# Performance work log

Measured on AMD Instinct MI355X. Metric: run time of the kernel, lower is better.

## Reference

```python
import jax, jax.numpy as jnp
import numpy as np

NUM_HEADS = 16
THETA = 10000.0


def _rope(x, cos, sin):
    # x: [B, H, S, d_k]; cos/sin: [S, d_k//2] broadcast over B, H
    x1 = x[..., 0::2]
    x2 = x[..., 1::2]
    r1 = cos * x1 - sin * x2
    r2 = sin * x1 + cos * x2
    # interleave back: (..., half_d, 2) -> (..., d_k)
    return jnp.stack((r1, r2), axis=-1).reshape(x.shape)


def setup_inputs() -> dict:
    key = jax.random.key(0)
    ks = jax.random.split(key, 5)
    B, S, D = 4, 2048, 1024
    scale = D ** -0.5
    x = jax.random.normal(ks[0], (B, S, D), dtype=jnp.float32)
    wq = jax.random.normal(ks[1], (D, D), dtype=jnp.float32) * scale
    wk = jax.random.normal(ks[2], (D, D), dtype=jnp.float32) * scale
    wv = jax.random.normal(ks[3], (D, D), dtype=jnp.float32) * scale
    wo = jax.random.normal(ks[4], (D, D), dtype=jnp.float32) * scale
    return {"x": x, "wq": wq, "wk": wk, "wv": wv, "wo": wo}


def reference(x, wq, wk, wv, wo):
    B, S, D = x.shape
    H = NUM_HEADS
    dk = D // H

    def proj(w):
        # x @ w.T, split heads -> [B, H, S, dk]
        y = jnp.einsum('bsd,ed->bse', x, w)
        return y.reshape(B, S, H, dk).transpose(0, 2, 1, 3)

    q, k, v = proj(wq), proj(wk), proj(wv)

    # RoPE (interleaved pairs), positions = arange(S)
    inv_freq = THETA ** (-(jnp.arange(0, dk, 2, dtype=jnp.float32) / dk))
    ang = jnp.arange(S, dtype=jnp.float32)[:, None] * inv_freq  # [S, dk//2]
    cos, sin = jnp.cos(ang), jnp.sin(ang)
    q = _rope(q, cos, sin)
    k = _rope(k, cos, sin)

    scores = jnp.einsum('bhqd,bhkd->bhqk', q, k) / jnp.sqrt(jnp.asarray(dk, x.dtype))
    causal = jnp.tril(jnp.ones((S, S), dtype=bool))  # keep self + past
    scores = jnp.where(causal, scores, -jnp.inf)
    p = jax.nn.softmax(scores, axis=-1)
    attn = jnp.einsum('bhqk,bhkd->bhqd', p, v)
    attn = attn.transpose(0, 2, 1, 3).reshape(B, S, D)
    return jnp.einsum('bsd,ed->bse', attn, wo)
```

## Files before the change

### kernel.cpp

```cpp
#include <hip/hip_runtime.h>
#include <hip/hip_bf16.h>
#include <cstdint>
#include <cstddef>

#define Bb 4
#define Ss 2048
#define Dd 1024
#define Hh 16
#define Mm (Bb*Ss)

typedef __bf16 bf16_t;
typedef __bf16 bf16x8 __attribute__((ext_vector_type(8)));
typedef __bf16 bf16x4 __attribute__((ext_vector_type(4)));
typedef float  f32x4  __attribute__((ext_vector_type(4)));
typedef float  f32x16 __attribute__((ext_vector_type(16)));
typedef unsigned int u32x4 __attribute__((ext_vector_type(4)));
typedef unsigned int u32x2 __attribute__((ext_vector_type(2)));

#define MFMA16(a,b,c) __builtin_amdgcn_mfma_f32_16x16x32_bf16(a,b,c,0,0,0)
#define MFMA32(a,b,c) __builtin_amdgcn_mfma_f32_32x32x16_bf16(a,b,c,0,0,0)

#define QSCALE 0.18033688011112042f

static __device__ __forceinline__ float fexp2(float x) {
#if __has_builtin(__builtin_amdgcn_exp2f)
  return __builtin_amdgcn_exp2f(x);
#else
  return exp2f(x);
#endif
}

static __device__ __forceinline__ bf16x8 ld16g(const bf16_t* p) {
  return __builtin_bit_cast(bf16x8, *reinterpret_cast<const u32x4*>(p));
}

static __device__ __forceinline__ void gload_lds16(const bf16_t* g, bf16_t* l) {
  __builtin_amdgcn_global_load_lds(
      (__attribute__((address_space(1))) void*)(g),
      (__attribute__((address_space(3))) void*)(l),
      16, 0, 0);
}

__global__ void prep_k(const float* __restrict__ x,  const float* __restrict__ wq,
                       const float* __restrict__ wk, const float* __restrict__ wv,
                       const float* __restrict__ wo,
                       bf16_t* __restrict__ xb, bf16_t* __restrict__ wqkv,
                       float2* __restrict__ tab) {
  int bid = blockIdx.x;
  if (bid < 8192) {
    int i = (bid * 256 + threadIdx.x) * 4;
    float4 f = *reinterpret_cast<const float4*>(x + i);
    xb[i + 0] = (bf16_t)f.x; xb[i + 1] = (bf16_t)f.y;
    xb[i + 2] = (bf16_t)f.z; xb[i + 3] = (bf16_t)f.w;
  } else if (bid < 12288) {
    int b2 = bid - 8192;
    int seg = b2 >> 10, local = b2 & 1023;
    const float* w = (seg == 0) ? wq : (seg == 1) ? wk : (seg == 2) ? wv : wo;
    int i = (local * 256 + threadIdx.x) * 4;
    float4 f = *reinterpret_cast<const float4*>(w + i);
    bf16_t* o = wqkv + (size_t)seg * (Dd * Dd) + i;
    o[0] = (bf16_t)f.x; o[1] = (bf16_t)f.y; o[2] = (bf16_t)f.z; o[3] = (bf16_t)f.w;
  } else {
    int idx = (bid - 12288) * 256 + threadIdx.x;
    int i = idx & 31, s = idx >> 5;
    float inv_freq = exp2f(-(float)i * (13.2877123795494f / 32.0f));
    float ang = (float)s * inv_freq;
    float sn, cs;
    sincosf(ang, &sn, &cs);
    tab[idx] = make_float2(cs, sn);
  }
}

template <typename OutT>
__global__ __launch_bounds__(256, 3) void gemm_r3(const bf16_t* __restrict__ A,
                                                  const bf16_t* __restrict__ Bm,
                                                  OutT* __restrict__ C0,
                                                  OutT* __restrict__ C1,
                                                  OutT* __restrict__ C2,
                                                  const float2* __restrict__ tab,
                                                  int Kdim) {
  __shared__ bf16_t As[3][128 * 32];
  __shared__ bf16_t Bs[3][128 * 32];
  const int t = threadIdx.x;
  const int lane = t & 63, w = t >> 6;
  const int l15 = lane & 15, lg = lane >> 4;
  const int wr = w >> 1, wc = w & 1;
  const int m0 = blockIdx.x * 128, n0 = blockIdx.y * 128;

  const bf16_t* gA[2];
  const bf16_t* gB[2];
#pragma unroll
  for (int i = 0; i < 2; ++i) {
    int q = i * 256 + t, row = q >> 2, sl = (q & 3) ^ ((row >> 1) & 3);
    gA[i] = A  + (size_t)(m0 + row) * Kdim + sl * 8;
    gB[i] = Bm + (size_t)(n0 + row) * Kdim + sl * 8;
  }
  const int wb = w * 64 * 8;

  auto stage = [&](int slot, int k0) {
#pragma unroll
    for (int i = 0; i < 2; ++i) {
      gload_lds16(gA[i] + k0, &As[slot][i * 2048 + wb]);
      gload_lds16(gB[i] + k0, &Bs[slot][i * 2048 + wb]);
    }
  };

  int aoff[4], boff[4];
#pragma unroll
  for (int i = 0; i < 4; ++i) {
    int row = wr * 64 + i * 16 + l15;
    aoff[i] = row * 32 + ((lg ^ ((row >> 1) & 3)) * 8);
  }
#pragma unroll
  for (int j = 0; j < 4; ++j) {
    int row = wc * 64 + j * 16 + l15;
    boff[j] = row * 32 + ((lg ^ ((row >> 1) & 3)) * 8);
  }

  f32x4 acc[4][4] = {};
  const int KT = Kdim / 32;

  stage(0, 0);
  stage(1, 32);
  for (int j = 0; j < KT; ++j) {
    if (j == KT - 1) {
      asm volatile("s_waitcnt vmcnt(0) lgkmcnt(0)" ::: "memory");
    } else {
      asm volatile("s_waitcnt vmcnt(4) lgkmcnt(0)" ::: "memory");
    }
    __builtin_amdgcn_s_barrier();
    if (j + 2 < KT) stage((j + 2) % 3, (j + 2) * 32);
    const bf16_t* ab = As[j % 3];
    const bf16_t* bb = Bs[j % 3];
    bf16x8 a[4], b[4];
#pragma unroll
    for (int jj = 0; jj < 4; ++jj)
      b[jj] = __builtin_bit_cast(bf16x8,
               *reinterpret_cast<const u32x4*>(bb + boff[jj]));
#pragma unroll
    for (int i = 0; i < 4; ++i)
      a[i] = __builtin_bit_cast(bf16x8,
               *reinterpret_cast<const u32x4*>(ab + aoff[i]));
    __builtin_amdgcn_s_setprio(1);
#pragma unroll
    for (int i = 0; i < 4; ++i)
#pragma unroll
      for (int jj = 0; jj < 4; ++jj)
        acc[i][jj] = MFMA16(a[i], b[jj], acc[i][jj]);
    __builtin_amdgcn_s_setprio(0);
  }

  OutT* Cs = (n0 < 1024) ? C0 : (n0 < 2048 ? C1 : C2);
  const int nb = n0 & 1023;
  const bool doRope = (tab != nullptr) && (n0 < 2048);
  const float qs = (n0 < 1024) ? QSCALE : 1.0f;

  if (doRope) {
#pragma unroll
    for (int i = 0; i < 4; ++i) {
      int rowb = m0 + wr * 64 + i * 16 + lg * 4;
#pragma unroll
      for (int j = 0; j < 4; ++j) {
        int col = nb + wc * 64 + j * 16 + l15;
        int i0 = (col & 63) >> 1;
        const bool ev = !(col & 1);
#pragma unroll
        for (int r = 0; r < 4; ++r) {
          float v = acc[i][j][r];
          float px = __shfl_xor(v, 1);
          int s = (rowb + r) & (Ss - 1);
          float2 f = tab[s * 32 + i0];
          float sn = ev ? -f.y : f.y;
          Cs[(size_t)(rowb + r) * 1024 + col] = (OutT)((f.x * v + sn * px) * qs);
        }
      }
    }
  } else {
#pragma unroll
    for (int i = 0; i < 4; ++i) {
      int rowb = m0 + wr * 64 + i * 16 + lg * 4;
#pragma unroll
      for (int j = 0; j < 4; ++j) {
        int col = nb + wc * 64 + j * 16 + l15;
#pragma unroll
        for (int r = 0; r < 4; ++r)
          Cs[(size_t)(rowb + r) * 1024 + col] = (OutT)acc[i][j][r];
      }
    }
  }
}

__global__ __launch_bounds__(256) void transpose_v(const bf16_t* __restrict__ V,
                                                   bf16_t* __restrict__ Vt) {
  __shared__ bf16_t tile[64][72];
  int bh = blockIdx.y;
  int b = bh >> 4, h = bh & 15;
  int s0 = blockIdx.x * 64;
  int t = threadIdx.x;
  const bf16_t* vbase = V + (size_t)b * Ss * Dd + h * 64;
#pragma unroll
  for (int c = 0; c < 2; ++c) {
    int cf = c * 256 + t;
    int s = cf >> 3, d8 = cf & 7;
    u32x4 v = *reinterpret_cast<const u32x4*>(vbase + (size_t)(s0 + s) * Dd + d8 * 8);
    *reinterpret_cast<u32x4*>(&tile[s][d8 * 8]) = v;
  }
  __syncthreads();
  bf16_t* obase = Vt + (size_t)bh * 64 * Ss;
#pragma unroll
  for (int c = 0; c < 2; ++c) {
    int cf = c * 256 + t;
    int d = cf >> 3, s8 = cf & 7;
    __align__(16) bf16_t tmp[8];
#pragma unroll
    for (int i = 0; i < 8; ++i) tmp[i] = tile[s8 * 8 + i][d];
    *reinterpret_cast<u32x4*>(obase + (size_t)d * Ss + s0 + s8 * 8) =
        *reinterpret_cast<const u32x4*>(tmp);
  }
}

__global__ __launch_bounds__(256, 2) void attn_k(const bf16_t* __restrict__ Q,
                                                 const bf16_t* __restrict__ K,
                                                 const bf16_t* __restrict__ Vt,
                                                 bf16_t* __restrict__ O) {
  __shared__ bf16_t Ks[3][4096];
  __shared__ bf16_t Vs[3][4096];
  const int t = threadIdx.x, lane = t & 63, w = t >> 6;
  const int l31 = lane & 31, hi = lane >> 5, hi8 = hi * 8;
  const int bh = blockIdx.y, b = bh >> 4, h = bh & 15;
  const int bx = blockIdx.x;
  const int i = bx * 4 + w;
  const int q0a = 32 * i, q0b = 2016 - 32 * i;
  const int dtA = q0a >> 6, hfA = (q0a >> 5) & 1;
  const int dtB = q0b >> 6, hfB = (q0b >> 5) & 1;
  const int NT = 32 - 2 * bx;
  const bf16_t* qb = Q + (size_t)b * Ss * Dd + h * 64;
  const bf16_t* kb = K + (size_t)b * Ss * Dd + h * 64;
  const bf16_t* vtb = Vt + (size_t)bh * 64 * Ss;

  const int a_ = l31 >> 2, c_ = l31 & 3;
  const int tau = (a_ >> 1) + 2 * (a_ & 1) + ((a_ & 4) >> 1);
  const int sig = c_ + 4 * tau;

  int kfoff[4];
#pragma unroll
  for (int c = 0; c < 4; ++c) {
    int j = sig >> 1, u = (sig & 1) * 8 + c * 2 + hi;
    kfoff[c] = j * 128 + ((u ^ j) * 8);
  }
  int vfoff[2][2];
#pragma unroll
  for (int db = 0; db < 2; ++db)
#pragma unroll
    for (int ks = 0; ks < 2; ++ks) {
      int d = db * 32 + l31, j = d >> 2, u = (d & 3) * 4 + ks * 2 + hi;
      vfoff[db][ks] = j * 128 + ((u ^ j) * 8);
    }

  const int sj = t >> 4, ss = t & 15, su = ss ^ sj;
  const bf16_t* ksrc0 = kb + (size_t)(2 * sj + (su >> 3)) * Dd + (su & 7) * 8;
  const bf16_t* vsrc0 = vtb + (size_t)(4 * sj + (su >> 2)) * Ss + (su & 3) * 8;

  auto stage = [&](int buf, int kb0) {
    bf16_t* kd = &Ks[buf][w * 512];
    bf16_t* vd = &Vs[buf][w * 512];
    gload_lds16(ksrc0 + (size_t)kb0 * Dd, kd);
    gload_lds16(ksrc0 + (size_t)(kb0 + 32) * Dd, kd + 2048);
    gload_lds16(vsrc0 + kb0, vd);
    gload_lds16(vsrc0 + kb0 + 32, vd + 2048);
  };

  bf16x8 qf[2][4];
#pragma unroll
  for (int c = 0; c < 4; ++c) {
    qf[0][c] = ld16g(qb + (size_t)(q0a + l31) * Dd + c * 16 + hi8);
    qf[1][c] = ld16g(qb + (size_t)(q0b + l31) * Dd + c * 16 + hi8);
  }

  float l_[2] = {0.f, 0.f};
  f32x16 o_[2][2] = {};

  auto chain = [&](int kt, int dt, int hf, bf16x8 (&qc)[4],
                   f32x16& o0, f32x16& o1, float& lc,
                   bf16x8 (&kf)[2][4], bf16x8 (&vf)[2][2][2]) {
    if (kt > dt) return;
    const bool last = (kt == dt);
    const bool do1 = !(last && hf == 0);
    f32x16 s0 = {}, s1 = {};
    __builtin_amdgcn_s_setprio(1);
    s0 = MFMA32(kf[0][0], qc[0], s0);
    s0 = MFMA32(kf[0][1], qc[1], s0);
    s0 = MFMA32(kf[0][2], qc[2], s0);
    s0 = MFMA32(kf[0][3], qc[3], s0);
    if (do1) {
      s1 = MFMA32(kf[1][0], qc[0], s1);
      s1 = MFMA32(kf[1][1], qc[1], s1);
      s1 = MFMA32(kf[1][2], qc[2], s1);
      s1 = MFMA32(kf[1][3], qc[3], s1);
    }
    __builtin_amdgcn_s_setprio(0);
    if (last) {
      if (hf) {
#pragma unroll
        for (int reg = 0; reg < 16; ++reg) {
          const int koff = (reg & 3) + 4 * (reg >> 2) + 8 * ((reg >> 2) >> 1) + hi8;
          s1[reg] = (koff <= l31) ? s1[reg] : -INFINITY;
        }
      } else {
#pragma unroll
        for (int reg = 0; reg < 16; ++reg) {
          const int koff = (reg & 3) + 4 * (reg >> 2) + 8 * ((reg >> 2) >> 1) + hi8;
          s0[reg] = (koff <= l31) ? s0[reg] : -INFINITY;
        }
      }
    }
    float p0[16], p1[16];
#pragma unroll
    for (int r = 0; r < 16; ++r) p0[r] = fexp2(s0[r]);
    bf16x8 pa0, pa1, pb0, pb1;
#pragma unroll
    for (int r = 0; r < 8; ++r) { pa0[r] = (bf16_t)p0[r]; pa1[r] = (bf16_t)p0[r + 8]; }
    if (do1) {
#pragma unroll
      for (int r = 0; r < 16; ++r) p1[r] = fexp2(s1[r]);
#pragma unroll
      for (int r = 0; r < 8; ++r) { pb0[r] = (bf16_t)p1[r]; pb1[r] = (bf16_t)p1[r + 8]; }
#pragma unroll
      for (int r = 0; r < 16; ++r) p0[r] += p1[r];
    }
#pragma unroll
    for (int st2 = 8; st2 > 0; st2 >>= 1)
#pragma unroll
      for (int r = 0; r < st2; ++r) p0[r] += p0[r + st2];
    lc += p0[0];
    __builtin_amdgcn_s_setprio(1);
    o0 = MFMA32(vf[0][0][0], pa0, o0);
    o0 = MFMA32(vf[0][0][1], pa1, o0);
    o1 = MFMA32(vf[0][1][0], pa0, o1);
    o1 = MFMA32(vf[0][1][1], pa1, o1);
    if (do1) {
      o0 = MFMA32(vf[1][0][0], pb0, o0);
      o0 = MFMA32(vf[1][0][1], pb1, o0);
      o1 = MFMA32(vf[1][1][0], pb0, o1);
      o1 = MFMA32(vf[1][1][1], pb1, o1);
    }
    __builtin_amdgcn_s_setprio(0);
  };

  stage(0, 0);
  stage(1, 64);
  for (int j = 0; j < NT; ++j) {
    if (j == NT - 1) {
      asm volatile("s_waitcnt vmcnt(0) lgkmcnt(0)" ::: "memory");
    } else {
      asm volatile("s_waitcnt vmcnt(4) lgkmcnt(0)" ::: "memory");
    }
    __builtin_amdgcn_s_barrier();
    if (j + 2 < NT) stage((j + 2) % 3, (j + 2) * 64);
    const bf16_t* kbuf = &Ks[j % 3][0];
    const bf16_t* vbuf = &Vs[j % 3][0];
    bf16x8 kf[2][4], vf[2][2][2];
#pragma unroll
    for (int st = 0; st < 2; ++st)
#pragma unroll
      for (int c = 0; c < 4; ++c)
        kf[st][c] = __builtin_bit_cast(bf16x8,
            *reinterpret_cast<const u32x4*>(kbuf + st * 2048 + kfoff[c]));
#pragma unroll
    for (int st = 0; st < 2; ++st)
#pragma unroll
      for (int db = 0; db < 2; ++db)
#pragma unroll
        for (int ks = 0; ks < 2; ++ks)
          vf[st][db][ks] = __builtin_bit_cast(bf16x8,
              *reinterpret_cast<const u32x4*>(vbuf + st * 2048 + vfoff[db][ks]));
    chain(j, dtA, hfA, qf[0], o_[0][0], o_[0][1], l_[0], kf, vf);
    chain(j, dtB, hfB, qf[1], o_[1][0], o_[1][1], l_[1], kf, vf);
  }

#pragma unroll
  for (int ch = 0; ch < 2; ++ch) {
    const float ltot = l_[ch] + __shfl_xor(l_[ch], 32);
    const float inv = 1.0f / ltot;
    const size_t rowoff = ((size_t)b * Ss + (ch ? q0b : q0a) + l31) * Dd + h * 64;
#pragma unroll
    for (int db = 0; db < 2; ++db)
#pragma unroll
      for (int tt = 0; tt < 4; ++tt) {
        bf16x4 ov;
#pragma unroll
        for (int c = 0; c < 4; ++c) ov[c] = (bf16_t)(o_[ch][db][4 * tt + c] * inv);
        *reinterpret_cast<u32x2*>(&O[rowoff + db * 32 + 8 * tt + 4 * hi]) =
            __builtin_bit_cast(u32x2, ov);
      }
  }
}

extern "C" void kernel_launch(void* const* d_in, const int* in_sizes, int n_in,
                              void* d_out, int out_size, void* d_ws, size_t ws_size,
                              hipStream_t stream) {
  (void)in_sizes; (void)n_in; (void)out_size; (void)ws_size;
  const float* x  = (const float*)d_in[0];
  const float* wq = (const float*)d_in[1];
  const float* wk = (const float*)d_in[2];
  const float* wv = (const float*)d_in[3];
  const float* wo = (const float*)d_in[4];
  float* out = (float*)d_out;

  char* ws = (char*)d_ws;
  const size_t MB16 = 16u << 20;
  bf16_t* xb   = (bf16_t*)(ws + 0);
  bf16_t* Qb   = (bf16_t*)(ws + 1 * MB16);
  bf16_t* Kb   = (bf16_t*)(ws + 2 * MB16);
  bf16_t* Vb   = (bf16_t*)(ws + 3 * MB16);
  bf16_t* wqkv = (bf16_t*)(ws + 4 * MB16);
  bf16_t* wob  = wqkv + 3u * Dd * Dd;
  float2* tab  = (float2*)(ws + 4 * MB16 + (8u << 20));
  bf16_t* Vt   = xb;
  bf16_t* AOb  = Vb;

  prep_k<<<12544, 256, 0, stream>>>(x, wq, wk, wv, wo, xb, wqkv, tab);

  gemm_r3<bf16_t><<<dim3(Mm / 128, 24), 256, 0, stream>>>(xb, wqkv, Qb, Kb, Vb,
                                                          tab, Dd);

  transpose_v<<<dim3(Ss / 64, Bb * Hh), 256, 0, stream>>>(Vb, Vt);

  attn_k<<<dim3(8, Bb * Hh), 256, 0, stream>>>(Qb, Kb, Vt, AOb);

  gemm_r3<float><<<dim3(Mm / 128, 8), 256, 0, stream>>>(AOb, wob, out, out, out,
                                                        nullptr, Dd);
}
```

Before: 173.4 us.

## Fuse V transpose into QKV GEMM epilogue and double-buffer 128-key attention tiles

The QKV GEMM now writes the V projection directly in transposed [B,H,d,S] layout from its epilogue, which removes the separate transpose kernel launch and its extra round trip through memory. The attention kernel moves from a triple-buffered 64-key pipeline to double-buffered 128-key stages, halving the number of barriers and waits per key range. The transposed epilogue writes are 8-byte strided stores, which may coalesce poorly. Waiting on vmcnt(0) each iteration also reduces how much load latency is overlapped with compute.

```diff
diff --git a/kernel.cpp b/kernel.cpp
--- a/kernel.cpp
+++ b/kernel.cpp
@@ -76,7 +76,7 @@
                                                   const bf16_t* __restrict__ Bm,
                                                   OutT* __restrict__ C0,
                                                   OutT* __restrict__ C1,
-                                                  OutT* __restrict__ C2,
+                                                  bf16_t* __restrict__ VtOut,
                                                   const float2* __restrict__ tab,
                                                   int Kdim) {
   __shared__ bf16_t As[3][128 * 32];
@@ -150,8 +150,27 @@
     __builtin_amdgcn_s_setprio(0);
   }
 
-  OutT* Cs = (n0 < 1024) ? C0 : (n0 < 2048 ? C1 : C2);
   const int nb = n0 & 1023;
+  if (VtOut != nullptr && n0 >= 2048) {
+#pragma unroll
+    for (int i = 0; i < 4; ++i) {
+      int rowb = m0 + wr * 64 + i * 16 + lg * 4;
+      int b = rowb >> 11, s = rowb & 2047;
+#pragma unroll
+      for (int j = 0; j < 4; ++j) {
+        int col = nb + wc * 64 + j * 16 + l15;
+        int h = col >> 6, d = col & 63;
+        bf16x4 ov;
+#pragma unroll
+        for (int r = 0; r < 4; ++r) ov[r] = (bf16_t)acc[i][j][r];
+        *reinterpret_cast<u32x2*>(
+            &VtOut[(((size_t)(b * 16 + h)) * 64 + d) * 2048 + s]) =
+            __builtin_bit_cast(u32x2, ov);
+      }
+    }
+    return;
+  }
+  OutT* Cs = (n0 < 1024) ? C0 : C1;
   const bool doRope = (tab != nullptr) && (n0 < 2048);
   const float qs = (n0 < 1024) ? QSCALE : 1.0f;
 
@@ -190,41 +209,12 @@
   }
 }
 
-__global__ __launch_bounds__(256) void transpose_v(const bf16_t* __restrict__ V,
-                                                   bf16_t* __restrict__ Vt) {
-  __shared__ bf16_t tile[64][72];
-  int bh = blockIdx.y;
-  int b = bh >> 4, h = bh & 15;
-  int s0 = blockIdx.x * 64;
-  int t = threadIdx.x;
-  const bf16_t* vbase = V + (size_t)b * Ss * Dd + h * 64;
-#pragma unroll
-  for (int c = 0; c < 2; ++c) {
-    int cf = c * 256 + t;
-    int s = cf >> 3, d8 = cf & 7;
-    u32x4 v = *reinterpret_cast<const u32x4*>(vbase + (size_t)(s0 + s) * Dd + d8 * 8);
-    *reinterpret_cast<u32x4*>(&tile[s][d8 * 8]) = v;
-  }
-  __syncthreads();
-  bf16_t* obase = Vt + (size_t)bh * 64 * Ss;
-#pragma unroll
-  for (int c = 0; c < 2; ++c) {
-    int cf = c * 256 + t;
-    int d = cf >> 3, s8 = cf & 7;
-    __align__(16) bf16_t tmp[8];
-#pragma unroll
-    for (int i = 0; i < 8; ++i) tmp[i] = tile[s8 * 8 + i][d];
-    *reinterpret_cast<u32x4*>(obase + (size_t)d * Ss + s0 + s8 * 8) =
-        *reinterpret_cast<const u32x4*>(tmp);
-  }
-}
-
 __global__ __launch_bounds__(256, 2) void attn_k(const bf16_t* __restrict__ Q,
                                                  const bf16_t* __restrict__ K,
                                                  const bf16_t* __restrict__ Vt,
                                                  bf16_t* __restrict__ O) {
-  __shared__ bf16_t Ks[3][4096];
-  __shared__ bf16_t Vs[3][4096];
+  __shared__ bf16_t Ks[2][8192];
+  __shared__ bf16_t Vs[2][8192];
   const int t = threadIdx.x, lane = t & 63, w = t >> 6;
   const int l31 = lane & 31, hi = lane >> 5, hi8 = hi * 8;
   const int bh = blockIdx.y, b = bh >> 4, h = bh & 15;
@@ -233,7 +223,7 @@
   const int q0a = 32 * i, q0b = 2016 - 32 * i;
   const int dtA = q0a >> 6, hfA = (q0a >> 5) & 1;
   const int dtB = q0b >> 6, hfB = (q0b >> 5) & 1;
-  const int NT = 32 - 2 * bx;
+  const int NT2 = 16 - bx;
   const bf16_t* qb = Q + (size_t)b * Ss * Dd + h * 64;
   const bf16_t* kb = K + (size_t)b * Ss * Dd + h * 64;
   const bf16_t* vtb = Vt + (size_t)bh * 64 * Ss;
@@ -261,13 +251,14 @@
   const bf16_t* ksrc0 = kb + (size_t)(2 * sj + (su >> 3)) * Dd + (su & 7) * 8;
   const bf16_t* vsrc0 = vtb + (size_t)(4 * sj + (su >> 2)) * Ss + (su & 3) * 8;
 
-  auto stage = [&](int buf, int kb0) {
+  auto stage128 = [&](int buf, int kb0) {
     bf16_t* kd = &Ks[buf][w * 512];
     bf16_t* vd = &Vs[buf][w * 512];
-    gload_lds16(ksrc0 + (size_t)kb0 * Dd, kd);
-    gload_lds16(ksrc0 + (size_t)(kb0 + 32) * Dd, kd + 2048);
-    gload_lds16(vsrc0 + kb0, vd);
-    gload_lds16(vsrc0 + kb0 + 32, vd + 2048);
+#pragma unroll
+    for (int st = 0; st < 4; ++st) {
+      gload_lds16(ksrc0 + (size_t)(kb0 + 32 * st) * Dd, kd + st * 2048);
+      gload_lds16(vsrc0 + kb0 + 32 * st,                vd + st * 2048);
+    }
   };
 
   bf16x8 qf[2][4];
@@ -347,35 +338,35 @@
     __builtin_amdgcn_s_setprio(0);
   };
 
-  stage(0, 0);
-  stage(1, 64);
-  for (int j = 0; j < NT; ++j) {
-    if (j == NT - 1) {
-      asm volatile("s_waitcnt vmcnt(0) lgkmcnt(0)" ::: "memory");
-    } else {
-      asm volatile("s_waitcnt vmcnt(4) lgkmcnt(0)" ::: "memory");
-    }
+  stage128(0, 0);
+  for (int jj = 0; jj < NT2; ++jj) {
+    asm volatile("s_waitcnt vmcnt(0) lgkmcnt(0)" ::: "memory");
     __builtin_amdgcn_s_barrier();
-    if (j + 2 < NT) stage((j + 2) % 3, (j + 2) * 64);
-    const bf16_t* kbuf = &Ks[j % 3][0];
-    const bf16_t* vbuf = &Vs[j % 3][0];
-    bf16x8 kf[2][4], vf[2][2][2];
-#pragma unroll
-    for (int st = 0; st < 2; ++st)
-#pragma unroll
-      for (int c = 0; c < 4; ++c)
-        kf[st][c] = __builtin_bit_cast(bf16x8,
-            *reinterpret_cast<const u32x4*>(kbuf + st * 2048 + kfoff[c]));
-#pragma unroll
-    for (int st = 0; st < 2; ++st)
-#pragma unroll
-      for (int db = 0; db < 2; ++db)
-#pragma unroll
-        for (int ks = 0; ks < 2; ++ks)
-          vf[st][db][ks] = __builtin_bit_cast(bf16x8,
-              *reinterpret_cast<const u32x4*>(vbuf + st * 2048 + vfoff[db][ks]));
-    chain(j, dtA, hfA, qf[0], o_[0][0], o_[0][1], l_[0], kf, vf);
-    chain(j, dtB, hfB, qf[1], o_[1][0], o_[1][1], l_[1], kf, vf);
+    if (jj + 1 < NT2) stage128((jj + 1) & 1, (jj + 1) * 128);
+    const bf16_t* kbuf = &Ks[jj & 1][0];
+    const bf16_t* vbuf = &Vs[jj & 1][0];
+#pragma unroll
+    for (int half = 0; half < 2; ++half) {
+      const int kt = 2 * jj + half;
+      const int base = half * 4096;
+      bf16x8 kf[2][4], vf[2][2][2];
+#pragma unroll
+      for (int st = 0; st < 2; ++st)
+#pragma unroll
+        for (int c = 0; c < 4; ++c)
+          kf[st][c] = __builtin_bit_cast(bf16x8,
+              *reinterpret_cast<const u32x4*>(kbuf + base + st * 2048 + kfoff[c]));
+#pragma unroll
+      for (int st = 0; st < 2; ++st)
+#pragma unroll
+        for (int db = 0; db < 2; ++db)
+#pragma unroll
+          for (int ks = 0; ks < 2; ++ks)
+            vf[st][db][ks] = __builtin_bit_cast(bf16x8,
+                *reinterpret_cast<const u32x4*>(vbuf + base + st * 2048 + vfoff[db][ks]));
+      chain(kt, dtA, hfA, qf[0], o_[0][0], o_[0][1], l_[0], kf, vf);
+      chain(kt, dtB, hfB, qf[1], o_[1][0], o_[1][1], l_[1], kf, vf);
+    }
   }
 
 #pragma unroll
@@ -412,22 +403,19 @@
   bf16_t* xb   = (bf16_t*)(ws + 0);
   bf16_t* Qb   = (bf16_t*)(ws + 1 * MB16);
   bf16_t* Kb   = (bf16_t*)(ws + 2 * MB16);
-  bf16_t* Vb   = (bf16_t*)(ws + 3 * MB16);
+  bf16_t* Vt   = (bf16_t*)(ws + 3 * MB16);
   bf16_t* wqkv = (bf16_t*)(ws + 4 * MB16);
   bf16_t* wob  = wqkv + 3u * Dd * Dd;
   float2* tab  = (float2*)(ws + 4 * MB16 + (8u << 20));
-  bf16_t* Vt   = xb;
-  bf16_t* AOb  = Vb;
+  bf16_t* AOb  = xb;
 
   prep_k<<<12544, 256, 0, stream>>>(x, wq, wk, wv, wo, xb, wqkv, tab);
 
-  gemm_r3<bf16_t><<<dim3(Mm / 128, 24), 256, 0, stream>>>(xb, wqkv, Qb, Kb, Vb,
+  gemm_r3<bf16_t><<<dim3(Mm / 128, 24), 256, 0, stream>>>(xb, wqkv, Qb, Kb, Vt,
                                                           tab, Dd);
 
-  transpose_v<<<dim3(Ss / 64, Bb * Hh), 256, 0, stream>>>(Vb, Vt);
-
   attn_k<<<dim3(8, Bb * Hh), 256, 0, stream>>>(Qb, Kb, Vt, AOb);
 
-  gemm_r3<float><<<dim3(Mm / 128, 8), 256, 0, stream>>>(AOb, wob, out, out, out,
-                                                        nullptr, Dd);
-}
+  gemm_r3<float><<<dim3(Mm / 128, 8), 256, 0, stream>>>(AOb, wob, out, out,
+                                                        nullptr, nullptr, Dd);
+}
```

New measurement: 164.8 us, median of 3. 1.05x faster.
